# Optimization experiments

Hardware: AMD Instinct MI355X
Metric: run time of the kernel (lower is better)

## Reference

```python
import jax, jax.numpy as jnp
import numpy as np

N, E, G = 100000, 1600000, 2000
D_IN, D_H, D_MLP, D_OUT = 768, 128, 32, 2


def setup_inputs() -> dict:
    key = jax.random.key(0)
    ks = jax.random.split(key, 12)
    x = jax.random.normal(ks[0], (N, D_IN), dtype=jnp.float32)
    edge_index = jax.random.randint(ks[1], (2, E), 0, N, dtype=jnp.int64)
    edge_attr = jax.random.uniform(ks[2], (E, 1), dtype=jnp.float32)
    batch = jnp.sort(jax.random.randint(ks[3], (N,), 0, G, dtype=jnp.int64))
    s1 = 1.0 / np.sqrt(D_IN)
    s2 = 1.0 / np.sqrt(D_H)
    s3 = 1.0 / np.sqrt(D_MLP)
    return {
        "x": x, "edge_index": edge_index, "edge_attr": edge_attr,
        "batch": batch, "num_graphs": G,
        "W1i": jax.random.normal(ks[4], (D_IN, D_H), dtype=jnp.float32) * s1,
        "W1r": jax.random.normal(ks[5], (D_IN, D_H), dtype=jnp.float32) * s1,
        "b1": jnp.zeros((D_H,), dtype=jnp.float32),
        "W2i": jax.random.normal(ks[6], (D_H, D_H), dtype=jnp.float32) * s2,
        "W2r": jax.random.normal(ks[7], (D_H, D_H), dtype=jnp.float32) * s2,
        "b2": jnp.zeros((D_H,), dtype=jnp.float32),
        "Wl1": jax.random.normal(ks[8], (D_H, D_MLP), dtype=jnp.float32) * s2,
        "bl1": jnp.zeros((D_MLP,), dtype=jnp.float32),
        "Wl2": jax.random.normal(ks[9], (D_MLP, D_OUT), dtype=jnp.float32) * s3,
        "bl2": jnp.zeros((D_OUT,), dtype=jnp.float32),
    }


def _arma_conv(x, row, col, ew, Wi, Wr, b, n_nodes):
    # gcn_norm without self-loops: D^{-1/2} A D^{-1/2}
    deg = jax.ops.segment_sum(ew, col, num_segments=n_nodes)
    dinv = jnp.where(deg > 0, jax.lax.rsqrt(jnp.where(deg > 0, deg, 1.0)), 0.0)
    norm = dinv[row] * ew * dinv[col]
    h = x @ Wi                                   # [N, F_out]
    msg = h[row] * norm[:, None]                 # gather + scale  [E, F_out]
    agg = jax.ops.segment_sum(msg, col, num_segments=n_nodes)
    return jax.nn.relu(agg + x @ Wr + b)         # ARMA: K=1, T=1, act=ReLU


def reference(x, edge_index, edge_attr, batch, num_graphs,
              W1i, W1r, b1, W2i, W2r, b2, Wl1, bl1, Wl2, bl2):
    row, col = edge_index[0], edge_index[1]
    ew = edge_attr.reshape(-1)
    n = x.shape[0]
    h = jax.nn.elu(_arma_conv(x, row, col, ew, W1i, W1r, b1, n))
    node_x = _arma_conv(h, row, col, ew, W2i, W2r, b2, n)
    # global mean pool over graphs
    sums = jax.ops.segment_sum(node_x, batch, num_segments=num_graphs)
    cnt = jax.ops.segment_sum(jnp.ones((n,), node_x.dtype), batch, num_segments=num_graphs)
    graph_x = sums / jnp.maximum(cnt, 1.0)[:, None]
    pred = jax.nn.elu(graph_x @ Wl1 + bl1) @ Wl2 + bl2
    return pred
```

## Files before the change

### kernel.cpp

```cpp
#include <hip/hip_runtime.h>
#include <hip/hip_bf16.h>
#include <math.h>

typedef __attribute__((ext_vector_type(8))) short short8;
typedef __attribute__((ext_vector_type(4))) float f32x4;
typedef __attribute__((ext_vector_type(2))) float f32x2;
typedef __attribute__((address_space(1))) const void gvoid;
typedef __attribute__((address_space(3))) void lvoid;

#define NC 8

__device__ __forceinline__ unsigned short f2bf(float f) {
    unsigned int u = __builtin_bit_cast(unsigned int, f);
    return (unsigned short)((u + 0x7fffu + ((u >> 16) & 1u)) >> 16);
}
__device__ __forceinline__ float b2f(short s) {
    return __builtin_bit_cast(float, ((unsigned int)(unsigned short)s) << 16);
}
__device__ __forceinline__ unsigned int cvtpk(float lo, float hi) {
    unsigned int r;
    asm("v_cvt_pk_bf16_f32 %0, %1, %2" : "=v"(r) : "v"(lo), "v"(hi));
    return r;
}
__device__ __forceinline__ unsigned int pk8_lo(float a, float b, unsigned int old) {
    return (unsigned int)__builtin_amdgcn_cvt_pk_fp8_f32(a, b, (int)old, false);
}
__device__ __forceinline__ unsigned int pk8_hi(float a, float b, unsigned int old) {
    return (unsigned int)__builtin_amdgcn_cvt_pk_fp8_f32(a, b, (int)old, true);
}
__device__ __forceinline__ f32x2 up8_lo(unsigned int v) {
    return __builtin_amdgcn_cvt_pk_f32_fp8((int)v, false);
}
__device__ __forceinline__ f32x2 up8_hi(unsigned int v) {
    return __builtin_amdgcn_cvt_pk_f32_fp8((int)v, true);
}
__device__ __forceinline__ void acc16(float* A, const uint4 u, const float n) {
    f32x2 p;
    p = up8_lo(u.x); A[0]  = fmaf(p.x, n, A[0]);  A[1]  = fmaf(p.y, n, A[1]);
    p = up8_hi(u.x); A[2]  = fmaf(p.x, n, A[2]);  A[3]  = fmaf(p.y, n, A[3]);
    p = up8_lo(u.y); A[4]  = fmaf(p.x, n, A[4]);  A[5]  = fmaf(p.y, n, A[5]);
    p = up8_hi(u.y); A[6]  = fmaf(p.x, n, A[6]);  A[7]  = fmaf(p.y, n, A[7]);
    p = up8_lo(u.z); A[8]  = fmaf(p.x, n, A[8]);  A[9]  = fmaf(p.y, n, A[9]);
    p = up8_hi(u.z); A[10] = fmaf(p.x, n, A[10]); A[11] = fmaf(p.y, n, A[11]);
    p = up8_lo(u.w); A[12] = fmaf(p.x, n, A[12]); A[13] = fmaf(p.y, n, A[13]);
    p = up8_hi(u.w); A[14] = fmaf(p.x, n, A[14]); A[15] = fmaf(p.y, n, A[15]);
}

__global__ __launch_bounds__(256) void hist_conv_kernel(
    const int* __restrict__ ei, const float* __restrict__ ea,
    unsigned long long* __restrict__ packed, int* __restrict__ rank, int N, int E,
    int eBlocks,
    const float* __restrict__ W1i, const float* __restrict__ W1r,
    const float* __restrict__ W2i, const float* __restrict__ W2r,
    unsigned short* __restrict__ W1t, unsigned short* __restrict__ W2t)
{
    if ((int)blockIdx.x < eBlocks) {
        int e = blockIdx.x * 256 + threadIdx.x;
        if (e >= E) return;
        const int copy = blockIdx.x & (NC - 1);
        int c = ei[(size_t)E + e];
        unsigned long long fx = (unsigned long long)(ea[e] * 1048576.0f + 0.5f);
        unsigned long long old = atomicAdd(&packed[(size_t)copy * N + c], (1ULL << 42) | fx);
        rank[e] = (int)(old >> 42);
    } else {
        int id = (blockIdx.x - eBlocks) * 256 + threadIdx.x;
        if (id < 256 * 768) {
            int n = id / 768, j = id % 768;
            int k = (j & ~63) | ((((j >> 3) & 7) ^ (n & 7)) << 3) | (j & 7);
            float v = (n < 128) ? W1i[k * 128 + n] : W1r[k * 128 + (n - 128)];
            W1t[id] = f2bf(v);
        } else {
            int id2 = id - 256 * 768;
            if (id2 < 128 * 256) {
                int n = id2 >> 8, j = id2 & 255;
                int k = (j & ~63) | ((((j >> 3) & 7) ^ (n & 7)) << 3) | (j & 7);
                float v = (k < 128) ? W2i[k * 128 + n] : W2r[(k - 128) * 128 + n];
                W2t[id2] = f2bf(v);
            }
        }
    }
}

__global__ __launch_bounds__(256) void scan1p_kernel(
    const unsigned long long* __restrict__ packed, int* __restrict__ out,
    int* __restrict__ blksum, int n)
{
    __shared__ int part[256];
    const int t = threadIdx.x;
    const int base = blockIdx.x * 1024 + t * 4;
    int v[4];
#pragma unroll
    for (int q = 0; q < 4; ++q) {
        int s = 0;
        if (base + q < n) {
#pragma unroll
            for (int p = 0; p < NC; ++p)
                s += (int)(packed[(size_t)p * n + base + q] >> 42);
        }
        v[q] = s;
    }
    const int s = v[0] + v[1] + v[2] + v[3];
    part[t] = s;
    __syncthreads();
    for (int off = 1; off < 256; off <<= 1) {
        int x = (t >= off) ? part[t - off] : 0;
        __syncthreads();
        part[t] += x;
        __syncthreads();
    }
    if (t == 255) blksum[blockIdx.x] = part[255];
    int run = part[t] - s;
#pragma unroll
    for (int q = 0; q < 4; ++q) {
        if (base + q < n) out[base + q] = run;
        run += v[q];
    }
}

__global__ __launch_bounds__(256) void scan3_kernel(
    int* __restrict__ rowptr, const int* __restrict__ blksum,
    int* __restrict__ wpb, const unsigned long long* __restrict__ packed,
    float* __restrict__ dinv, int n, int Etot, int nb)
{
    __shared__ int tmp[256];
    __shared__ int sexcl[256];
    const int t = threadIdx.x;
    const int v = (t < nb) ? blksum[t] : 0;
    tmp[t] = v;
    __syncthreads();
    for (int off = 1; off < 256; off <<= 1) {
        int x = (t >= off) ? tmp[t - off] : 0;
        __syncthreads();
        tmp[t] += x;
        __syncthreads();
    }
    sexcl[t] = tmp[t] - v;
    __syncthreads();
    const int i = blockIdx.x * 256 + t;
    if (i == 0) rowptr[n] = Etot;
    if (i >= n) return;
    int base = rowptr[i] + sexcl[i >> 10];
    rowptr[i] = base;
    unsigned long long degfx = 0;
    int acc = base;
#pragma unroll
    for (int p = 0; p < NC; ++p) {
        unsigned long long vv = packed[(size_t)p * n + i];
        wpb[(size_t)p * n + i] = acc;
        acc += (int)(vv >> 42);
        degfx += vv & ((1ULL << 42) - 1);
    }
    dinv[i] = (degfx > 0) ? rsqrtf((float)degfx * 9.5367431640625e-7f) : 0.f;
}

__global__ __launch_bounds__(512) void gemm1_place_kernel(
    const float* __restrict__ A, const unsigned short* __restrict__ Wt,
    const float* __restrict__ bias, unsigned char* __restrict__ outP8,
    unsigned short* __restrict__ outR, int M, int K, int gB,
    const int* __restrict__ ei, const float* __restrict__ ea,
    const float* __restrict__ dinv, const int* __restrict__ wpb,
    const int* __restrict__ rank, int2* __restrict__ csr, int E)
{
    __shared__ __align__(16) unsigned char As[64 * 128];
    __shared__ __align__(16) unsigned char Bs[256 * 128];

    if ((int)blockIdx.x >= gB) {
        int e = (blockIdx.x - gB) * 512 + threadIdx.x;
        if (e >= E) return;
        const int copy = (e >> 8) & (NC - 1);
        int r = ei[e];
        int c = ei[(size_t)E + e];
        float nm = dinv[r] * ea[e] * dinv[c];
        int pos = wpb[(size_t)copy * M + c] + rank[e];
        int2 rec;
        rec.x = r;
        rec.y = __builtin_bit_cast(int, nm);
        csr[pos] = rec;
        return;
    }

    const int t = threadIdx.x;
    const int m0 = blockIdx.x * 64;
    const int lane = t & 63;
    const int wid = t >> 6;
    const int wm = wid >> 2;
    const int wn = wid & 3;
    const int lr = lane & 15;
    const int lk = (lane >> 4) * 8;

    f32x4 acc[2][4] = {};

    const int sr = t >> 3;
    const int sk = (t & 7) * 8;
    const int aRow = m0 + sr;
    const bool aOk = (aRow < M);
    const float* aSrc = A + (size_t)(aOk ? aRow : 0) * K + sk;
    const int aDst = sr * 128 + ((sk * 2) ^ ((sr & 7) << 4));
    const unsigned short* bSrc = Wt + (size_t)(lane >> 3) * K + (lane & 7) * 8;

    for (int k0 = 0; k0 < K; k0 += 64) {
#pragma unroll
        for (int i = 0; i < 4; ++i) {
            const int chunk = i * 8 + wid;
            __builtin_amdgcn_global_load_lds(
                (gvoid*)(bSrc + (size_t)chunk * 8 * K + k0),
                (lvoid*)(Bs + chunk * 1024), 16, 0, 0);
        }
        unsigned int p0 = 0, p1 = 0, p2 = 0, p3 = 0;
        if (aOk) {
            const float4 f0 = *(const float4*)(aSrc + k0);
            const float4 f1 = *(const float4*)(aSrc + k0 + 4);
            p0 = cvtpk(f0.x, f0.y);
            p1 = cvtpk(f0.z, f0.w);
            p2 = cvtpk(f1.x, f1.y);
            p3 = cvtpk(f1.z, f1.w);
        }
        uint4 uv = {p0, p1, p2, p3};
        *(uint4*)(As + aDst) = uv;
        __syncthreads();
#pragma unroll
        for (int ks = 0; ks < 2; ++ks) {
            short8 a[2], b[4];
#pragma unroll
            for (int mf = 0; mf < 2; ++mf) {
                const int r = wm * 32 + mf * 16 + lr;
                a[mf] = *(const short8*)(As + r * 128 + (((ks * 32 + lk) * 2) ^ ((r & 7) << 4)));
            }
#pragma unroll
            for (int nf = 0; nf < 4; ++nf) {
                const int n = wn * 64 + nf * 16 + lr;
                b[nf] = *(const short8*)(Bs + n * 128 + (((ks * 32 + lk) * 2) ^ ((n & 7) << 4)));
            }
#pragma unroll
            for (int mf = 0; mf < 2; ++mf)
#pragma unroll
                for (int nf = 0; nf < 4; ++nf)
                    acc[mf][nf] = __builtin_amdgcn_mfma_f32_16x16x32_bf16(
                        a[mf], b[nf], acc[mf][nf], 0, 0, 0);
        }
        __syncthreads();
    }

#pragma unroll
    for (int mf = 0; mf < 2; ++mf) {
#pragma unroll
        for (int nf = 0; nf < 4; ++nf) {
            const int n = wn * 64 + nf * 16 + lr;
            const f32x4 v = acc[mf][nf];
            const int mb = m0 + wm * 32 + mf * 16 + (lane >> 4) * 4;
            if (n < 128) {
                const unsigned int u01 = pk8_lo(v[0], v[1], 0u);
                const unsigned int u23 = pk8_lo(v[2], v[3], 0u);
                if (mb + 0 < M) outP8[(size_t)(mb + 0) * 128 + n] = (unsigned char)(u01);
                if (mb + 1 < M) outP8[(size_t)(mb + 1) * 128 + n] = (unsigned char)(u01 >> 8);
                if (mb + 2 < M) outP8[(size_t)(mb + 2) * 128 + n] = (unsigned char)(u23);
                if (mb + 3 < M) outP8[(size_t)(mb + 3) * 128 + n] = (unsigned char)(u23 >> 8);
            } else {
                const int nl = n - 128;
                const float badd = bias[nl];
#pragma unroll
                for (int j = 0; j < 4; ++j) {
                    if (mb + j < M) outR[(size_t)(mb + j) * 128 + nl] = f2bf(v[j] + badd);
                }
            }
        }
    }
}

__global__ __launch_bounds__(512) void gemm_mfma_single(
    const unsigned short* __restrict__ Aa,
    const unsigned short* __restrict__ Ah,
    const unsigned short* __restrict__ Wt,
    const float* __restrict__ bias,
    unsigned short* __restrict__ outX, int M)
{
    __shared__ __align__(16) unsigned char As[128 * 128];
    __shared__ __align__(16) unsigned char Bs[128 * 128];

    const int t = threadIdx.x;
    const int m0 = blockIdx.x * 128;
    const int lane = t & 63;
    const int wid = t >> 6;
    const int wm = wid >> 1;
    const int wn = wid & 1;
    const int lr = lane & 15;
    const int lk = (lane >> 4) * 8;

    f32x4 acc[2][4] = {};

    const int sr = t >> 2;
    const int sk = (t & 3) * 16;
    const int aRow = m0 + sr;
    const bool aOk = (aRow < M);
    const int rowSafe = aOk ? aRow : 0;
    const int sw = (sr & 7) << 4;
    const unsigned short* bSrc = Wt + (size_t)(lane >> 3) * 256 + (lane & 7) * 8;

    for (int k0 = 0; k0 < 256; k0 += 64) {
#pragma unroll
        for (int i = 0; i < 2; ++i) {
            const int chunk = i * 8 + wid;
            __builtin_amdgcn_global_load_lds(
                (gvoid*)(bSrc + (size_t)chunk * 8 * 256 + k0),
                (lvoid*)(Bs + chunk * 1024), 16, 0, 0);
        }
        const unsigned short* src =
            (k0 < 128 ? Aa : Ah) + (size_t)rowSafe * 128 + (k0 & 127) + sk;
        const short8 v0 = *(const short8*)(src);
        const short8 v1 = *(const short8*)(src + 8);
        *(short8*)(As + sr * 128 + ((sk * 2) ^ sw)) = v0;
        *(short8*)(As + sr * 128 + ((sk * 2 + 16) ^ sw)) = v1;
        __syncthreads();
#pragma unroll
        for (int ks = 0; ks < 2; ++ks) {
            short8 a[2], b[4];
#pragma unroll
            for (int mf = 0; mf < 2; ++mf) {
                const int r = wm * 32 + mf * 16 + lr;
                a[mf] = *(const short8*)(As + r * 128 + (((ks * 32 + lk) * 2) ^ ((r & 7) << 4)));
            }
#pragma unroll
            for (int nf = 0; nf < 4; ++nf) {
                const int n = wn * 64 + nf * 16 + lr;
                b[nf] = *(const short8*)(Bs + n * 128 + (((ks * 32 + lk) * 2) ^ ((n & 7) << 4)));
            }
#pragma unroll
            for (int mf = 0; mf < 2; ++mf)
#pragma unroll
                for (int nf = 0; nf < 4; ++nf)
                    acc[mf][nf] = __builtin_amdgcn_mfma_f32_16x16x32_bf16(
                        a[mf], b[nf], acc[mf][nf], 0, 0, 0);
        }
        __syncthreads();
    }

#pragma unroll
    for (int mf = 0; mf < 2; ++mf) {
#pragma unroll
        for (int nf = 0; nf < 4; ++nf) {
            const int n = wn * 64 + nf * 16 + lr;
            const float bb = bias[n];
            const f32x4 v = acc[mf][nf];
#pragma unroll
            for (int j = 0; j < 4; ++j) {
                const int m = m0 + wm * 32 + mf * 16 + (lane >> 4) * 4 + j;
                if (m < M) outX[(size_t)m * 128 + n] = f2bf(fmaxf(v[j] + bb, 0.f));
            }
        }
    }
}

__global__ __launch_bounds__(256) void agg_bias_relu(
    const unsigned char* __restrict__ P8, const unsigned short* __restrict__ Rbf,
    const int* __restrict__ rowptr, const int2* __restrict__ csr,
    unsigned short* __restrict__ hout, unsigned char* __restrict__ h8out, int N)
{
    const int i = blockIdx.x * 32 + (threadIdx.x >> 3);
    const int l = threadIdx.x & 7;
    if (i >= N) return;
    const int beg = rowptr[i];
    const int end = rowptr[i + 1];
    const int c = l * 16;

    float A0[16] = {}, A1[16] = {};
    int j = beg;
    for (; j + 1 < end; j += 2) {
        const int2 e0 = csr[j], e1 = csr[j + 1];
        const uint4 u0 = *(const uint4*)(P8 + (size_t)e0.x * 128 + c);
        const uint4 u1 = *(const uint4*)(P8 + (size_t)e1.x * 128 + c);
        acc16(A0, u0, __builtin_bit_cast(float, e0.y));
        acc16(A1, u1, __builtin_bit_cast(float, e1.y));
    }
    if (j < end) {
        const int2 e0 = csr[j];
        const uint4 u0 = *(const uint4*)(P8 + (size_t)e0.x * 128 + c);
        acc16(A0, u0, __builtin_bit_cast(float, e0.y));
    }
    const short8 r0 = *(const short8*)(Rbf + (size_t)i * 128 + c);
    const short8 r1 = *(const short8*)(Rbf + (size_t)i * 128 + c + 8);
    float s[16];
    short8 o0, o1;
#pragma unroll
    for (int q = 0; q < 8; ++q) {
        s[q] = fmaxf(A0[q] + A1[q] + b2f(r0[q]), 0.f);
        o0[q] = (short)f2bf(s[q]);
    }
#pragma unroll
    for (int q = 8; q < 16; ++q) {
        s[q] = fmaxf(A0[q] + A1[q] + b2f(r1[q - 8]), 0.f);
        o1[q - 8] = (short)f2bf(s[q]);
    }
    *(short8*)(hout + (size_t)i * 128 + c) = o0;
    *(short8*)(hout + (size_t)i * 128 + c + 8) = o1;
    uint4 w;
    w.x = pk8_hi(s[2],  s[3],  pk8_lo(s[0],  s[1],  0u));
    w.y = pk8_hi(s[6],  s[7],  pk8_lo(s[4],  s[5],  0u));
    w.z = pk8_hi(s[10], s[11], pk8_lo(s[8],  s[9],  0u));
    w.w = pk8_hi(s[14], s[15], pk8_lo(s[12], s[13], 0u));
    *(uint4*)(h8out + (size_t)i * 128 + c) = w;
}

__global__ __launch_bounds__(256) void agg_plain(
    const unsigned char* __restrict__ H8,
    const int* __restrict__ rowptr, const int2* __restrict__ csr,
    unsigned short* __restrict__ ahout, int N)
{
    const int i = blockIdx.x * 32 + (threadIdx.x >> 3);
    const int l = threadIdx.x & 7;
    if (i >= N) return;
    const int beg = rowptr[i];
    const int end = rowptr[i + 1];
    const int c = l * 16;

    float A0[16] = {}, A1[16] = {};
    int j = beg;
    for (; j + 1 < end; j += 2) {
        const int2 e0 = csr[j], e1 = csr[j + 1];
        const uint4 u0 = *(const uint4*)(H8 + (size_t)e0.x * 128 + c);
        const uint4 u1 = *(const uint4*)(H8 + (size_t)e1.x * 128 + c);
        acc16(A0, u0, __builtin_bit_cast(float, e0.y));
        acc16(A1, u1, __builtin_bit_cast(float, e1.y));
    }
    if (j < end) {
        const int2 e0 = csr[j];
        const uint4 u0 = *(const uint4*)(H8 + (size_t)e0.x * 128 + c);
        acc16(A0, u0, __builtin_bit_cast(float, e0.y));
    }
    short8 o0, o1;
#pragma unroll
    for (int q = 0; q < 8; ++q)  o0[q] = (short)f2bf(A0[q] + A1[q]);
#pragma unroll
    for (int q = 8; q < 16; ++q) o1[q - 8] = (short)f2bf(A0[q] + A1[q]);
    *(short8*)(ahout + (size_t)i * 128 + c) = o0;
    *(short8*)(ahout + (size_t)i * 128 + c + 8) = o1;
}

__global__ __launch_bounds__(256) void pool_mlp(
    const unsigned short* __restrict__ nx, const int* __restrict__ batch, int N,
    const float* __restrict__ Wl1, const float* __restrict__ bl1,
    const float* __restrict__ Wl2, const float* __restrict__ bl2,
    float* __restrict__ out)
{
    __shared__ float gxp[4][128];
    __shared__ float hid[32];
    __shared__ int rng[2];
    const int g = blockIdx.x;
    const int t = threadIdx.x;
    if (t < 2) {
        const int target = g + t;
        int lo = 0, hi = N;
        while (lo < hi) {
            int mid = (lo + hi) >> 1;
            if (batch[mid] < target) lo = mid + 1; else hi = mid;
        }
        rng[t] = lo;
    }
    __syncthreads();
    const int s = rng[0], e = rng[1];
    const int pr = t & 63;
    const int strm = t >> 6;
    float a0 = 0.f, b0 = 0.f, a1 = 0.f, b1 = 0.f;
    int i = s + strm;
    for (; i + 4 < e; i += 8) {
        const unsigned int u = *(const unsigned int*)&nx[(size_t)i * 128 + pr * 2];
        const unsigned int v = *(const unsigned int*)&nx[(size_t)(i + 4) * 128 + pr * 2];
        a0 += b2f((short)(u & 0xffff)); b0 += b2f((short)(u >> 16));
        a1 += b2f((short)(v & 0xffff)); b1 += b2f((short)(v >> 16));
    }
    if (i < e) {
        const unsigned int u = *(const unsigned int*)&nx[(size_t)i * 128 + pr * 2];
        a0 += b2f((short)(u & 0xffff)); b0 += b2f((short)(u >> 16));
    }
    gxp[strm][pr * 2] = a0 + a1;
    gxp[strm][pr * 2 + 1] = b0 + b1;
    __syncthreads();
    if (t < 128) {
        gxp[0][t] = ((gxp[0][t] + gxp[1][t]) + (gxp[2][t] + gxp[3][t]))
                    / fmaxf((float)(e - s), 1.f);
    }
    __syncthreads();
    if (t < 32) {
        float a = bl1[t];
#pragma unroll 8
        for (int k = 0; k < 128; ++k) a = fmaf(gxp[0][k], Wl1[k * 32 + t], a);
        hid[t] = a > 0.f ? a : expm1f(a);
    }
    __syncthreads();
    if (t < 2) {
        float a = bl2[t];
#pragma unroll
        for (int k = 0; k < 32; ++k) a = fmaf(hid[k], Wl2[k * 2 + t], a);
        out[(size_t)g * 2 + t] = a;
    }
}

extern "C" void kernel_launch(void* const* d_in, const int* in_sizes, int n_in,
                              void* d_out, int out_size, void* d_ws, size_t ws_size,
                              hipStream_t stream)
{
    const float* x     = (const float*)d_in[0];
    const int*   ei    = (const int*)d_in[1];
    const float* ea    = (const float*)d_in[2];
    const int*   batch = (const int*)d_in[3];
    const float* W1i   = (const float*)d_in[5];
    const float* W1r   = (const float*)d_in[6];
    const float* b1    = (const float*)d_in[7];
    const float* W2i   = (const float*)d_in[8];
    const float* W2r   = (const float*)d_in[9];
    const float* b2    = (const float*)d_in[10];
    const float* Wl1   = (const float*)d_in[11];
    const float* bl1   = (const float*)d_in[12];
    const float* Wl2   = (const float*)d_in[13];
    const float* bl2   = (const float*)d_in[14];

    const int N = in_sizes[0] / 768;
    const int E = in_sizes[2];
    const int G = out_size / 2;

    char* ws = (char*)d_ws;
    size_t off = 0;
    auto alloc = [&](size_t bytes) -> char* {
        char* p = ws + off;
        off = (off + bytes + 255) & ~(size_t)255;
        return p;
    };
    unsigned long long* packed = (unsigned long long*)alloc((size_t)NC * N * 8);
    int*   rank    = (int*)alloc((size_t)E * 4);
    int*   wpb     = (int*)alloc((size_t)NC * N * 4);
    float* dinv    = (float*)alloc((size_t)N * 4);
    int*   rowptr  = (int*)alloc((size_t)(N + 1) * 4);
    int*   blksum  = (int*)alloc((size_t)256 * 4);
    int2*  csr     = (int2*)alloc((size_t)E * 8);
    unsigned char*  P8   = (unsigned char*)alloc((size_t)N * 128);
    unsigned char*  H8   = (unsigned char*)alloc((size_t)N * 128);
    unsigned short* R1   = (unsigned short*)alloc((size_t)N * 128 * 2);
    unsigned short* hbf  = (unsigned short*)alloc((size_t)N * 128 * 2);
    unsigned short* ahb  = (unsigned short*)alloc((size_t)N * 128 * 2);
    unsigned short* nxb  = (unsigned short*)alloc((size_t)N * 128 * 2);
    unsigned short* W1t  = (unsigned short*)alloc((size_t)256 * 768 * 2);
    unsigned short* W2t  = (unsigned short*)alloc((size_t)128 * 256 * 2);

    const int eBlocks = (E + 255) / 256;
    const int cBlocks = (256 * 768 + 128 * 256 + 255) / 256;
    const int nb      = (N + 1023) / 1024;
    const int nBlocks = (N + 255) / 256;
    const int aBlocks = (N + 31) / 32;
    const int gB      = (N + 63) / 64;
    const int pB      = (E + 511) / 512;

    (void)hipMemsetAsync(packed, 0, (size_t)NC * N * 8, stream);
    hist_conv_kernel<<<eBlocks + cBlocks, 256, 0, stream>>>(
        ei, ea, packed, rank, N, E, eBlocks, W1i, W1r, W2i, W2r, W1t, W2t);
    scan1p_kernel<<<nb, 256, 0, stream>>>(packed, rowptr, blksum, N);
    scan3_kernel<<<nBlocks, 256, 0, stream>>>(rowptr, blksum, wpb, packed, dinv, N, E, nb);

    gemm1_place_kernel<<<gB + pB, 512, 0, stream>>>(
        x, W1t, b1, P8, R1, N, 768, gB, ei, ea, dinv, wpb, rank, csr, E);

    agg_bias_relu<<<aBlocks, 256, 0, stream>>>(P8, R1, rowptr, csr, hbf, H8, N);

    agg_plain<<<aBlocks, 256, 0, stream>>>(H8, rowptr, csr, ahb, N);
    gemm_mfma_single<<<(N + 127) / 128, 512, 0, stream>>>(ahb, hbf, W2t, b2, nxb, N);

    pool_mlp<<<G, 256, 0, stream>>>(nxb, batch, N, Wl1, bl1, Wl2, bl2, (float*)d_out);
}
```

Before: 371.4 us.

## Double-buffer A tile and prefetch next K-slice in gemm1 mainloop

The layer-1 GEMM mainloop now double-buffers the A tile in LDS. It issues the global loads of the next 64-wide K slice before the MFMA work on the current slice, then converts and stores them into the alternate buffer afterward. The goal is to hide the global-load latency of the fp32 A stream behind the matrix math. The B tile stays single-buffered and is still refilled after a barrier. This costs more LDS and live registers, and the second barrier still serialises the B loads.

```diff
diff --git a/kernel.cpp b/kernel.cpp
--- a/kernel.cpp
+++ b/kernel.cpp
@@ -161,7 +161,7 @@
     const float* __restrict__ dinv, const int* __restrict__ wpb,
     const int* __restrict__ rank, int2* __restrict__ csr, int E)
 {
-    __shared__ __align__(16) unsigned char As[64 * 128];
+    __shared__ __align__(16) unsigned char As[2][64 * 128];
     __shared__ __align__(16) unsigned char Bs[256 * 128];
 
     if ((int)blockIdx.x >= gB) {
@@ -198,33 +198,44 @@
     const int aDst = sr * 128 + ((sk * 2) ^ ((sr & 7) << 4));
     const unsigned short* bSrc = Wt + (size_t)(lane >> 3) * K + (lane & 7) * 8;
 
-    for (int k0 = 0; k0 < K; k0 += 64) {
-#pragma unroll
-        for (int i = 0; i < 4; ++i) {
-            const int chunk = i * 8 + wid;
-            __builtin_amdgcn_global_load_lds(
-                (gvoid*)(bSrc + (size_t)chunk * 8 * K + k0),
-                (lvoid*)(Bs + chunk * 1024), 16, 0, 0);
-        }
-        unsigned int p0 = 0, p1 = 0, p2 = 0, p3 = 0;
-        if (aOk) {
-            const float4 f0 = *(const float4*)(aSrc + k0);
-            const float4 f1 = *(const float4*)(aSrc + k0 + 4);
-            p0 = cvtpk(f0.x, f0.y);
-            p1 = cvtpk(f0.z, f0.w);
-            p2 = cvtpk(f1.x, f1.y);
-            p3 = cvtpk(f1.z, f1.w);
-        }
-        uint4 uv = {p0, p1, p2, p3};
-        *(uint4*)(As + aDst) = uv;
-        __syncthreads();
+    const int NIT = K >> 6;
+
+#pragma unroll
+    for (int i = 0; i < 4; ++i) {
+        const int chunk = i * 8 + wid;
+        __builtin_amdgcn_global_load_lds(
+            (gvoid*)(bSrc + (size_t)chunk * 8 * K),
+            (lvoid*)(Bs + chunk * 1024), 16, 0, 0);
+    }
+    {
+        float4 f0 = {}, f1 = {};
+        if (aOk) { f0 = *(const float4*)(aSrc); f1 = *(const float4*)(aSrc + 4); }
+        uint4 uv = {cvtpk(f0.x, f0.y), cvtpk(f0.z, f0.w),
+                    cvtpk(f1.x, f1.y), cvtpk(f1.z, f1.w)};
+        *(uint4*)(&As[0][aDst]) = uv;
+    }
+
+    for (int it = 0; it < NIT; ++it) {
+        const int cur = it & 1;
+        const int nxt = cur ^ 1;
+        const bool hasNext = (it + 1 < NIT);
+        const int k1 = (it + 1) << 6;
+
+        __syncthreads();
+
+        float4 g0 = {}, g1 = {};
+        if (hasNext && aOk) {
+            g0 = *(const float4*)(aSrc + k1);
+            g1 = *(const float4*)(aSrc + k1 + 4);
+        }
+
 #pragma unroll
         for (int ks = 0; ks < 2; ++ks) {
             short8 a[2], b[4];
 #pragma unroll
             for (int mf = 0; mf < 2; ++mf) {
                 const int r = wm * 32 + mf * 16 + lr;
-                a[mf] = *(const short8*)(As + r * 128 + (((ks * 32 + lk) * 2) ^ ((r & 7) << 4)));
+                a[mf] = *(const short8*)(&As[cur][r * 128 + (((ks * 32 + lk) * 2) ^ ((r & 7) << 4))]);
             }
 #pragma unroll
             for (int nf = 0; nf < 4; ++nf) {
@@ -238,7 +249,24 @@
                     acc[mf][nf] = __builtin_amdgcn_mfma_f32_16x16x32_bf16(
                         a[mf], b[nf], acc[mf][nf], 0, 0, 0);
         }
-        __syncthreads();
+
+        if (hasNext) {
+            uint4 uv = {cvtpk(g0.x, g0.y), cvtpk(g0.z, g0.w),
+                        cvtpk(g1.x, g1.y), cvtpk(g1.z, g1.w)};
+            *(uint4*)(&As[nxt][aDst]) = uv;
+        }
+
+        __syncthreads();
+
+        if (hasNext) {
+#pragma unroll
+            for (int i = 0; i < 4; ++i) {
+                const int chunk = i * 8 + wid;
+                __builtin_amdgcn_global_load_lds(
+                    (gvoid*)(bSrc + (size_t)chunk * 8 * K + k1),
+                    (lvoid*)(Bs + chunk * 1024), 16, 0, 0);
+            }
+        }
     }
 
 #pragma unroll
```

New measurement: 374.7 us. About the same (+0.9%).

## Stage 256-wide K slab of A per iteration with wider contiguous loads

Applied to the files above, without the earlier changes.

The first-layer GEMM now loads a 256-column slab of the fp32 activation row per thread group. Each thread issues eight float4 loads of 128 contiguous bytes. The slab is converted to bf16 and stored into four LDS tiles before looping over four 64-wide K steps, replacing one 32-byte load per thread per 64-wide step. This is meant to improve global read efficiency and memory-level parallelism on the dominant x stream. In exchange it uses four times the A shared memory (32 KB more), which may lower occupancy, and raises register pressure.

```diff
diff --git a/kernel.cpp b/kernel.cpp
--- a/kernel.cpp
+++ b/kernel.cpp
@@ -161,7 +161,7 @@
     const float* __restrict__ dinv, const int* __restrict__ wpb,
     const int* __restrict__ rank, int2* __restrict__ csr, int E)
 {
-    __shared__ __align__(16) unsigned char As[64 * 128];
+    __shared__ __align__(16) unsigned char As[4][64 * 128];
     __shared__ __align__(16) unsigned char Bs[256 * 128];
 
     if ((int)blockIdx.x >= gB) {
@@ -190,55 +190,66 @@
 
     f32x4 acc[2][4] = {};
 
-    const int sr = t >> 3;
-    const int sk = (t & 7) * 8;
+    const int sr  = t >> 3;
+    const int lr8 = t & 7;
+    const int ktl = lr8 >> 1;
+    const int kh  = lr8 & 1;
     const int aRow = m0 + sr;
     const bool aOk = (aRow < M);
-    const float* aSrc = A + (size_t)(aOk ? aRow : 0) * K + sk;
-    const int aDst = sr * 128 + ((sk * 2) ^ ((sr & 7) << 4));
+    const float* aSrc = A + (size_t)(aOk ? aRow : 0) * K + lr8 * 32;
+    const int swz = (sr & 7) << 4;
     const unsigned short* bSrc = Wt + (size_t)(lane >> 3) * K + (lane & 7) * 8;
 
-    for (int k0 = 0; k0 < K; k0 += 64) {
-#pragma unroll
-        for (int i = 0; i < 4; ++i) {
-            const int chunk = i * 8 + wid;
-            __builtin_amdgcn_global_load_lds(
-                (gvoid*)(bSrc + (size_t)chunk * 8 * K + k0),
-                (lvoid*)(Bs + chunk * 1024), 16, 0, 0);
-        }
-        unsigned int p0 = 0, p1 = 0, p2 = 0, p3 = 0;
-        if (aOk) {
-            const float4 f0 = *(const float4*)(aSrc + k0);
-            const float4 f1 = *(const float4*)(aSrc + k0 + 4);
-            p0 = cvtpk(f0.x, f0.y);
-            p1 = cvtpk(f0.z, f0.w);
-            p2 = cvtpk(f1.x, f1.y);
-            p3 = cvtpk(f1.z, f1.w);
-        }
-        uint4 uv = {p0, p1, p2, p3};
-        *(uint4*)(As + aDst) = uv;
-        __syncthreads();
-#pragma unroll
-        for (int ks = 0; ks < 2; ++ks) {
-            short8 a[2], b[4];
-#pragma unroll
-            for (int mf = 0; mf < 2; ++mf) {
-                const int r = wm * 32 + mf * 16 + lr;
-                a[mf] = *(const short8*)(As + r * 128 + (((ks * 32 + lk) * 2) ^ ((r & 7) << 4)));
-            }
-#pragma unroll
-            for (int nf = 0; nf < 4; ++nf) {
-                const int n = wn * 64 + nf * 16 + lr;
-                b[nf] = *(const short8*)(Bs + n * 128 + (((ks * 32 + lk) * 2) ^ ((n & 7) << 4)));
-            }
-#pragma unroll
-            for (int mf = 0; mf < 2; ++mf)
-#pragma unroll
-                for (int nf = 0; nf < 4; ++nf)
-                    acc[mf][nf] = __builtin_amdgcn_mfma_f32_16x16x32_bf16(
-                        a[mf], b[nf], acc[mf][nf], 0, 0, 0);
-        }
-        __syncthreads();
+    for (int kg = 0; kg < K; kg += 256) {
+        {
+            float4 f[8];
+#pragma unroll
+            for (int q = 0; q < 8; ++q)
+                f[q] = aOk ? *(const float4*)(aSrc + kg + q * 4)
+                           : float4{0.f, 0.f, 0.f, 0.f};
+#pragma unroll
+            for (int j = 0; j < 4; ++j) {
+                uint4 uv;
+                uv.x = cvtpk(f[2 * j].x, f[2 * j].y);
+                uv.y = cvtpk(f[2 * j].z, f[2 * j].w);
+                uv.z = cvtpk(f[2 * j + 1].x, f[2 * j + 1].y);
+                uv.w = cvtpk(f[2 * j + 1].z, f[2 * j + 1].w);
+                const int g = kh * 4 + j;
+                *(uint4*)(&As[ktl][sr * 128 + ((g * 16) ^ swz)]) = uv;
+            }
+        }
+        for (int kt = 0; kt < 4; ++kt) {
+            const int k0 = kg + kt * 64;
+#pragma unroll
+            for (int i = 0; i < 4; ++i) {
+                const int chunk = i * 8 + wid;
+                __builtin_amdgcn_global_load_lds(
+                    (gvoid*)(bSrc + (size_t)chunk * 8 * K + k0),
+                    (lvoid*)(Bs + chunk * 1024), 16, 0, 0);
+            }
+            __syncthreads();
+#pragma unroll
+            for (int ks = 0; ks < 2; ++ks) {
+                short8 a[2], b[4];
+#pragma unroll
+                for (int mf = 0; mf < 2; ++mf) {
+                    const int r = wm * 32 + mf * 16 + lr;
+                    a[mf] = *(const short8*)(&As[kt][r * 128 + (((ks * 32 + lk) * 2) ^ ((r & 7) << 4))]);
+                }
+#pragma unroll
+                for (int nf = 0; nf < 4; ++nf) {
+                    const int n = wn * 64 + nf * 16 + lr;
+                    b[nf] = *(const short8*)(Bs + n * 128 + (((ks * 32 + lk) * 2) ^ ((n & 7) << 4)));
+                }
+#pragma unroll
+                for (int mf = 0; mf < 2; ++mf)
+#pragma unroll
+                    for (int nf = 0; nf < 4; ++nf)
+                        acc[mf][nf] = __builtin_amdgcn_mfma_f32_16x16x32_bf16(
+                            a[mf], b[nf], acc[mf][nf], 0, 0, 0);
+            }
+            __syncthreads();
+        }
     }
 
 #pragma unroll
```

After: 401.1 us. 8.0% more time.
